# Performance work log

Measured on AMD Instinct MI355X. Metric: run time of the kernel, lower is better.

Reference implementation:

```python
import jax, jax.numpy as jnp
import numpy as np

B, N, D, H, PD, HID = 16, 512, 512, 8, 9, 32
DH = D // H


def setup_inputs() -> dict:
    key = jax.random.key(0)
    ks = jax.random.split(key, 8)
    h = jax.random.normal(ks[0], (B, N, D), dtype=jnp.float32)
    v = jax.random.normal(ks[1], (B, N, 4), dtype=jnp.float32)
    m = jax.random.randint(ks[2], (B, N), 0, 2, dtype=jnp.int32)
    token_type_ids = jax.random.randint(ks[3], (N,), 0, 4, dtype=jnp.int32)
    s = 1.0 / np.sqrt(D)
    W_qkv = jax.random.normal(ks[4], (D, 3 * D), dtype=jnp.float32) * s
    W_out = jax.random.normal(ks[5], (D, D), dtype=jnp.float32) * s
    W1 = jax.random.normal(ks[6], (PD, HID), dtype=jnp.float32) * (1.0 / np.sqrt(PD))
    b1 = jnp.zeros((HID,), dtype=jnp.float32)
    W2 = jax.random.normal(ks[7], (HID, H), dtype=jnp.float32) * (1.0 / np.sqrt(HID))
    b2 = jnp.zeros((H,), dtype=jnp.float32)
    return {"h": h, "v": v, "m": m, "token_type_ids": token_type_ids,
            "W_qkv": W_qkv, "W_out": W_out, "W1": W1, "b1": b1, "W2": W2, "b2": b2}


def build_pairwise_features(v, token_type_ids):
    # v: [B,N,4] -> e: [B,N,N,9] = [v_i - v_j (4), v_i * v_j (4), same_type (1)]
    vi = v[:, :, None, :]
    vj = v[:, None, :, :]
    same = (token_type_ids[:, None] == token_type_ids[None, :]).astype(v.dtype)
    same = jnp.broadcast_to(same[None, :, :, None], v.shape[:1] + same.shape + (1,))
    return jnp.concatenate([vi - vj, vi * vj, same], axis=-1)


def reference(h, v, m, token_type_ids, W_qkv, W_out, W1, b1, W2, b2):
    Bq, Nq, Dq = h.shape
    qkv = h @ W_qkv                                    # [B,N,3D]
    q, k, vv = jnp.split(qkv, 3, axis=-1)
    def heads(x):
        return x.reshape(Bq, Nq, H, DH).transpose(0, 2, 1, 3)  # [B,H,N,dh]
    q, k, vv = heads(q), heads(k), heads(vv)
    logits = jnp.einsum('bhid,bhjd->bhij', q, k) / jnp.sqrt(jnp.float32(DH))
    e = build_pairwise_features(v, token_type_ids)     # [B,N,N,9]
    bias = jax.nn.relu(e @ W1 + b1) @ W2 + b2          # [B,N,N,H]
    logits = logits + bias.transpose(0, 3, 1, 2)       # [B,H,N,N]
    key_invalid = (m == 0)[:, None, None, :]           # [B,1,1,N]
    logits = jnp.where(key_invalid, -jnp.inf, logits)
    attn = jax.nn.softmax(logits, axis=-1)             # dropout is identity (p=0/eval)
    out = jnp.einsum('bhij,bhjd->bhid', attn, vv)
    out = out.transpose(0, 2, 1, 3).reshape(Bq, Nq, Dq) @ W_out
    out = out * (m != 0).astype(out.dtype)[:, :, None]
    return out
```

## Files before the change

kernel.cpp:

```cpp
#include <hip/hip_runtime.h>
#include <hip/hip_bf16.h>
#include <hip/hip_fp16.h>

#define NN 512
#define HH 8
#define DHH 64

typedef __attribute__((ext_vector_type(8))) short short8v;
typedef __attribute__((ext_vector_type(8))) unsigned short ushort8v;
typedef __attribute__((ext_vector_type(4))) unsigned short ushort4v;
typedef __attribute__((ext_vector_type(4))) float f32x4;
typedef __attribute__((ext_vector_type(8))) _Float16 f16x8;
typedef __attribute__((ext_vector_type(4))) _Float16 f16x4;

__device__ __forceinline__ unsigned short f2bf(float x) {
  unsigned u = __builtin_bit_cast(unsigned, x);
  u += 0x7FFFu + ((u >> 16) & 1u);
  return (unsigned short)(u >> 16);
}
__device__ __forceinline__ int swz64(int r, int cb) { return r * 64 + (cb ^ (((r >> 1) & 3) << 4)); }
__device__ __forceinline__ int swz128(int r, int cb) { return r * 128 + (cb ^ ((r & 7) << 4)); }

__global__ __launch_bounds__(256) void cvt_bf(const float* __restrict__ src,
                                              unsigned short* __restrict__ dst, int n) {
  int i = (blockIdx.x * 256 + threadIdx.x) * 4;
  if (i < n) {
    float4 v = *(const float4*)&src[i];
    ushort4v o;
    o[0] = f2bf(v.x); o[1] = f2bf(v.y); o[2] = f2bf(v.z); o[3] = f2bf(v.w);
    *(ushort4v*)&dst[i] = o;
  }
}

__global__ __launch_bounds__(256) void transpose_cvt(const float* __restrict__ src,
                                                     unsigned short* __restrict__ dst,
                                                     int R, int C) {
  __shared__ float t[32][33];
  const int r0 = blockIdx.x * 32, c0 = blockIdx.y * 32;
  const int rr = threadIdx.x >> 3, c4 = (threadIdx.x & 7) * 4;
  float4 v = *(const float4*)&src[(size_t)(r0 + rr) * C + c0 + c4];
  t[rr][c4 + 0] = v.x; t[rr][c4 + 1] = v.y; t[rr][c4 + 2] = v.z; t[rr][c4 + 3] = v.w;
  __syncthreads();
  ushort4v o;
#pragma unroll
  for (int e = 0; e < 4; ++e) o[e] = f2bf(t[c4 + e][rr]);
  *(ushort4v*)&dst[(size_t)(c0 + rr) * R + r0 + c4] = o;
}

__device__ __forceinline__ void gemm128_body(const unsigned short* __restrict__ A,
                                             const unsigned short* __restrict__ Bt,
                                             int ldk, int m0, int n0,
                                             f32x4 acc[4][4], unsigned char* smem) {
  const int tid = threadIdx.x, lane = tid & 63, wid = tid >> 6;
  const int wm = wid >> 1, wn = wid & 1;
  int aoff[4], boff[4];
#pragma unroll
  for (int i = 0; i < 4; ++i) {
    aoff[i] = swz64(wm * 64 + i * 16 + (lane & 15), (lane >> 4) * 16);
    boff[i] = 8192 + swz64(wn * 64 + i * 16 + (lane & 15), (lane >> 4) * 16);
  }
  for (int k0 = 0; k0 < ldk; k0 += 32) {
#pragma unroll
    for (int p = 0; p < 2; ++p) {
      const int idx = p * 256 + tid;
      const int r = idx >> 2, cg = idx & 3;
      ushort8v av = *(const ushort8v*)&A[(size_t)(m0 + r) * ldk + k0 + cg * 8];
      *(ushort8v*)&smem[swz64(r, cg * 16)] = av;
      ushort8v bv = *(const ushort8v*)&Bt[(size_t)(n0 + r) * ldk + k0 + cg * 8];
      *(ushort8v*)&smem[8192 + swz64(r, cg * 16)] = bv;
    }
    __syncthreads();
    short8v a[4], b[4];
#pragma unroll
    for (int i = 0; i < 4; ++i) {
      a[i] = *(const short8v*)&smem[aoff[i]];
      b[i] = *(const short8v*)&smem[boff[i]];
    }
#pragma unroll
    for (int i = 0; i < 4; ++i)
#pragma unroll
      for (int j = 0; j < 4; ++j)
        acc[i][j] = __builtin_amdgcn_mfma_f32_16x16x32_bf16(a[i], b[j], acc[i][j], 0, 0, 0);
    __syncthreads();
  }
}

__global__ __launch_bounds__(256) void gemm_qkv(const unsigned short* __restrict__ A,
                                                const unsigned short* __restrict__ Bt,
                                                unsigned short* __restrict__ q,
                                                unsigned short* __restrict__ k,
                                                unsigned short* __restrict__ v) {
  __shared__ unsigned char smem[16384];
  f32x4 acc[4][4];
  const f32x4 z = {0.f, 0.f, 0.f, 0.f};
#pragma unroll
  for (int i = 0; i < 4; ++i)
#pragma unroll
    for (int j = 0; j < 4; ++j) acc[i][j] = z;
  gemm128_body(A, Bt, 512, blockIdx.x * 128, blockIdx.y * 128, acc, smem);
  const int lane = threadIdx.x & 63, wid = threadIdx.x >> 6;
  const int wm = wid >> 1, wn = wid & 1;
#pragma unroll
  for (int i = 0; i < 4; ++i) {
    const int row0 = blockIdx.x * 128 + wm * 64 + i * 16 + ((lane >> 4) << 2);
#pragma unroll
    for (int j = 0; j < 4; ++j) {
      const int col = blockIdx.y * 128 + wn * 64 + j * 16 + (lane & 15);
      const int part = col >> 9, head = (col >> 6) & 7, dh = col & 63;
      unsigned short* dst = (part == 0) ? q : ((part == 1) ? k : v);
#pragma unroll
      for (int rr = 0; rr < 4; ++rr) {
        const int row = row0 + rr;
        const int b_ = row >> 9, n_ = row & 511;
        dst[(((b_ * HH + head) * NN) + n_) * DHH + dh] = f2bf(acc[i][j][rr]);
      }
    }
  }
}

__global__ __launch_bounds__(256) void gemm_out(const unsigned short* __restrict__ A,
                                                const unsigned short* __restrict__ Bt,
                                                const int* __restrict__ msk,
                                                float* __restrict__ out) {
  __shared__ unsigned char smem[16384];
  f32x4 acc[4][4];
  const f32x4 z = {0.f, 0.f, 0.f, 0.f};
#pragma unroll
  for (int i = 0; i < 4; ++i)
#pragma unroll
    for (int j = 0; j < 4; ++j) acc[i][j] = z;
  gemm128_body(A, Bt, 512, blockIdx.x * 128, blockIdx.y * 128, acc, smem);
  const int lane = threadIdx.x & 63, wid = threadIdx.x >> 6;
  const int wm = wid >> 1, wn = wid & 1;
#pragma unroll
  for (int i = 0; i < 4; ++i) {
    const int row0 = blockIdx.x * 128 + wm * 64 + i * 16 + ((lane >> 4) << 2);
#pragma unroll
    for (int j = 0; j < 4; ++j) {
      const int col = blockIdx.y * 128 + wn * 64 + j * 16 + (lane & 15);
#pragma unroll
      for (int rr = 0; rr < 4; ++rr) {
        const int row = row0 + rr;
        const float mm = (msk[row] != 0) ? 1.f : 0.f;
        out[(size_t)row * 512 + col] = acc[i][j][rr] * mm;
      }
    }
  }
}

__global__ __launch_bounds__(256) void bias_mlp_mfma(
    const float* __restrict__ v, const int* __restrict__ tti,
    const float* __restrict__ W1, const float* __restrict__ b1,
    const float* __restrict__ W2, const float* __restrict__ b2,
    __half* __restrict__ bias) {
  __shared__ float sv[NN][4];
  __shared__ int stt[NN];
  __shared__ _Float16 hbuf[4][16 * 40];
  const int tid = threadIdx.x, lane = tid & 63, w = tid >> 6;
  const int i = blockIdx.x, b = blockIdx.y;
  const int l16 = lane & 15, lg = lane >> 4;
  for (int idx = tid; idx < NN; idx += 256) {
    *(float4*)&sv[idx][0] = *(const float4*)&v[(b * NN + idx) * 4];
    stt[idx] = tti[idx];
  }
  f16x8 w1f[2], w2f;
#pragma unroll
  for (int t = 0; t < 2; ++t)
#pragma unroll
    for (int e = 0; e < 8; ++e) {
      const int kk = lg * 8 + e;
      w1f[t][e] = (kk < 9) ? (_Float16)W1[kk * 32 + t * 16 + l16] : (_Float16)0.f;
    }
#pragma unroll
  for (int e = 0; e < 8; ++e)
    w2f[e] = (l16 < 8) ? (_Float16)W2[(lg * 8 + e) * 8 + l16] : (_Float16)0.f;
  const float b1v0 = b1[l16], b1v1 = b1[16 + l16];
  const float b2v = (l16 < 8) ? b2[l16] : 0.f;
  __syncthreads();
  const float4 vi = *(const float4*)&sv[i][0];
  const int ti = stt[i];
  _Float16* hb = &hbuf[w][0];
  for (int j0 = w * 16; j0 < NN; j0 += 64) {
    const int j = j0 + l16;
    const float4 vj = *(const float4*)&sv[j][0];
    f16x8 af = {0, 0, 0, 0, 0, 0, 0, 0};
    if (lg == 0) {
      af[0] = (_Float16)(vi.x - vj.x); af[1] = (_Float16)(vi.y - vj.y);
      af[2] = (_Float16)(vi.z - vj.z); af[3] = (_Float16)(vi.w - vj.w);
      af[4] = (_Float16)(vi.x * vj.x); af[5] = (_Float16)(vi.y * vj.y);
      af[6] = (_Float16)(vi.z * vj.z); af[7] = (_Float16)(vi.w * vj.w);
    } else if (lg == 1) {
      af[0] = (ti == stt[j]) ? (_Float16)1.f : (_Float16)0.f;
    }
    f32x4 h0 = {b1v0, b1v0, b1v0, b1v0};
    f32x4 h1 = {b1v1, b1v1, b1v1, b1v1};
    h0 = __builtin_amdgcn_mfma_f32_16x16x32_f16(af, w1f[0], h0, 0, 0, 0);
    h1 = __builtin_amdgcn_mfma_f32_16x16x32_f16(af, w1f[1], h1, 0, 0, 0);
#pragma unroll
    for (int r = 0; r < 4; ++r) {
      const int row = lg * 4 + r;
      hb[row * 40 + l16] = (_Float16)fmaxf(h0[r], 0.f);
      hb[row * 40 + 16 + l16] = (_Float16)fmaxf(h1[r], 0.f);
    }
    f16x8 af2 = *(const f16x8*)&hb[l16 * 40 + lg * 8];
    f32x4 o = {b2v, b2v, b2v, b2v};
    o = __builtin_amdgcn_mfma_f32_16x16x32_f16(af2, w2f, o, 0, 0, 0);
    if (l16 < 8) {
      f16x4 pk;
#pragma unroll
      for (int r = 0; r < 4; ++r) pk[r] = (_Float16)o[r];
      *(f16x4*)&bias[((size_t)(b * HH + l16) * NN + i) * NN + j0 + lg * 4] = pk;
    }
  }
}

__global__ __launch_bounds__(256) void attn_mfma(
    const unsigned short* __restrict__ q, const unsigned short* __restrict__ k,
    const unsigned short* __restrict__ v, const __half* __restrict__ bias,
    const int* __restrict__ msk, unsigned short* __restrict__ ao) {
  __shared__ unsigned char vt[8192];
  __shared__ unsigned char ps[4][2048];
  __shared__ float smask[NN];
  const int tid = threadIdx.x, lane = tid & 63, w = tid >> 6;
  const int it = blockIdx.x, h_ = blockIdx.y, b_ = blockIdx.z;
  const int bh = b_ * HH + h_;
  const unsigned short* qb = q + ((size_t)bh * NN + it * 64) * DHH;
  const unsigned short* kb = k + (size_t)bh * NN * DHH;
  const unsigned short* vb = v + (size_t)bh * NN * DHH;
  const __half* bb = bias + (size_t)bh * NN * NN;
  for (int j = tid; j < NN; j += 256) smask[j] = (msk[b_ * NN + j] != 0) ? 0.f : -1e30f;
  short8v qf[2];
#pragma unroll
  for (int kc = 0; kc < 2; ++kc)
    qf[kc] = *(const short8v*)&qb[(w * 16 + (lane & 15)) * DHH + kc * 32 + (lane >> 4) * 8];
  f32x4 acc[4];
  const f32x4 z = {0.f, 0.f, 0.f, 0.f};
#pragma unroll
  for (int d = 0; d < 4; ++d) acc[d] = z;
  float mrow[4], lrow[4];
#pragma unroll
  for (int r = 0; r < 4; ++r) { mrow[r] = -1e30f; lrow[r] = 0.f; }
  __syncthreads();
  const int irow_base = it * 64 + w * 16 + ((lane >> 4) << 2);
  for (int j0 = 0; j0 < NN; j0 += 64) {
#pragma unroll
    for (int p = 0; p < 2; ++p) {
      const int idx = p * 256 + tid;
      const int j = idx & 63, dh0 = (idx >> 6) * 8;
      ushort8v v8 = *(const ushort8v*)&vb[(j0 + j) * DHH + dh0];
#pragma unroll
      for (int e = 0; e < 8; ++e)
        *(unsigned short*)&vt[swz128(dh0 + e, 2 * j)] = v8[e];
    }
    f32x4 s[4];
#pragma unroll
    for (int jt = 0; jt < 4; ++jt) {
      const unsigned short* kr = &kb[(j0 + jt * 16 + (lane & 15)) * DHH + (lane >> 4) * 8];
      short8v kf0 = *(const short8v*)&kr[0];
      short8v kf1 = *(const short8v*)&kr[32];
      f32x4 t = z;
      t = __builtin_amdgcn_mfma_f32_16x16x32_bf16(qf[0], kf0, t, 0, 0, 0);
      t = __builtin_amdgcn_mfma_f32_16x16x32_bf16(qf[1], kf1, t, 0, 0, 0);
      s[jt] = t;
    }
#pragma unroll
    for (int jt = 0; jt < 4; ++jt) {
      const int jcol = j0 + jt * 16 + (lane & 15);
#pragma unroll
      for (int r = 0; r < 4; ++r) {
        const float bv = __half2float(bb[(size_t)(irow_base + r) * NN + jcol]);
        s[jt][r] = fmaf(s[jt][r], 0.125f, bv) + smask[jcol];
      }
    }
    float alpha[4];
#pragma unroll
    for (int r = 0; r < 4; ++r) {
      float tm = fmaxf(fmaxf(s[0][r], s[1][r]), fmaxf(s[2][r], s[3][r]));
      tm = fmaxf(tm, __shfl_xor(tm, 1));
      tm = fmaxf(tm, __shfl_xor(tm, 2));
      tm = fmaxf(tm, __shfl_xor(tm, 4));
      tm = fmaxf(tm, __shfl_xor(tm, 8));
      const float mn = fmaxf(mrow[r], tm);
      alpha[r] = __expf(mrow[r] - mn);
      mrow[r] = mn;
      float ts = 0.f;
#pragma unroll
      for (int jt = 0; jt < 4; ++jt) {
        const float p = __expf(s[jt][r] - mn);
        s[jt][r] = p;
        ts += p;
      }
      ts += __shfl_xor(ts, 1);
      ts += __shfl_xor(ts, 2);
      ts += __shfl_xor(ts, 4);
      ts += __shfl_xor(ts, 8);
      lrow[r] = lrow[r] * alpha[r] + ts;
    }
#pragma unroll
    for (int d = 0; d < 4; ++d)
#pragma unroll
      for (int r = 0; r < 4; ++r) acc[d][r] *= alpha[r];
#pragma unroll
    for (int jt = 0; jt < 4; ++jt)
#pragma unroll
      for (int r = 0; r < 4; ++r)
        *(unsigned short*)&ps[w][swz128(((lane >> 4) << 2) + r, jt * 32 + 2 * (lane & 15))] =
            f2bf(s[jt][r]);
    __syncthreads();
    short8v pf[2];
#pragma unroll
    for (int kc = 0; kc < 2; ++kc)
      pf[kc] = *(const short8v*)&ps[w][swz128(lane & 15, kc * 64 + (lane >> 4) * 16)];
#pragma unroll
    for (int d = 0; d < 4; ++d) {
      short8v vf0 = *(const short8v*)&vt[swz128(d * 16 + (lane & 15), (lane >> 4) * 16)];
      short8v vf1 = *(const short8v*)&vt[swz128(d * 16 + (lane & 15), 64 + (lane >> 4) * 16)];
      acc[d] = __builtin_amdgcn_mfma_f32_16x16x32_bf16(pf[0], vf0, acc[d], 0, 0, 0);
      acc[d] = __builtin_amdgcn_mfma_f32_16x16x32_bf16(pf[1], vf1, acc[d], 0, 0, 0);
    }
    __syncthreads();
  }
#pragma unroll
  for (int d = 0; d < 4; ++d) {
#pragma unroll
    for (int r = 0; r < 4; ++r) {
      const int row = irow_base + r;
      ao[(size_t)(b_ * NN + row) * 512 + h_ * DHH + d * 16 + (lane & 15)] =
          f2bf(acc[d][r] / lrow[r]);
    }
  }
}

extern "C" void kernel_launch(void* const* d_in, const int* in_sizes, int n_in,
                              void* d_out, int out_size, void* d_ws, size_t ws_size,
                              hipStream_t stream) {
  const float* h     = (const float*)d_in[0];
  const float* v     = (const float*)d_in[1];
  const int*   m     = (const int*)d_in[2];
  const int*   tti   = (const int*)d_in[3];
  const float* W_qkv = (const float*)d_in[4];
  const float* W_out = (const float*)d_in[5];
  const float* W1    = (const float*)d_in[6];
  const float* b1    = (const float*)d_in[7];
  const float* W2    = (const float*)d_in[8];
  const float* b2    = (const float*)d_in[9];
  float* out = (float*)d_out;
  unsigned char* ws = (unsigned char*)d_ws;

  unsigned short* h_bf  = (unsigned short*)(ws + 0);
  unsigned short* q_bf  = (unsigned short*)(ws + 8388608);
  unsigned short* k_bf  = (unsigned short*)(ws + 16777216);
  unsigned short* v_bf  = (unsigned short*)(ws + 25165824);
  unsigned short* ao_bf = (unsigned short*)(ws + 33554432);
  unsigned short* WqT   = (unsigned short*)(ws + 41943040);
  unsigned short* WoT   = (unsigned short*)(ws + 43515904);
  __half* bias          = (__half*)(ws + 44040192);

  cvt_bf<<<4096, 256, 0, stream>>>(h, h_bf, 16 * NN * 512);
  transpose_cvt<<<dim3(16, 48), 256, 0, stream>>>(W_qkv, WqT, 512, 1536);
  transpose_cvt<<<dim3(16, 16), 256, 0, stream>>>(W_out, WoT, 512, 512);
  gemm_qkv<<<dim3(64, 12), 256, 0, stream>>>(h_bf, WqT, q_bf, k_bf, v_bf);
  bias_mlp_mfma<<<dim3(512, 16), 256, 0, stream>>>(v, tti, W1, b1, W2, b2, bias);
  attn_mfma<<<dim3(8, 8, 16), 256, 0, stream>>>(q_bf, k_bf, v_bf, bias, m, ao_bf);
  gemm_out<<<dim3(64, 4), 256, 0, stream>>>(ao_bf, WoT, m, out);
}
```

Measured before the change: 151.3 us.

## Fuse pairwise bias MLP into attention kernel and store V transposed

```diff
diff --git a/kernel.cpp b/kernel.cpp
--- a/kernel.cpp
+++ b/kernel.cpp
@@ -89,7 +89,7 @@
                                                 const unsigned short* __restrict__ Bt,
                                                 unsigned short* __restrict__ q,
                                                 unsigned short* __restrict__ k,
-                                                unsigned short* __restrict__ v) {
+                                                unsigned short* __restrict__ vt) {
   __shared__ unsigned char smem[16384];
   f32x4 acc[4][4];
   const f32x4 z = {0.f, 0.f, 0.f, 0.f};
@@ -107,12 +107,17 @@
     for (int j = 0; j < 4; ++j) {
       const int col = blockIdx.y * 128 + wn * 64 + j * 16 + (lane & 15);
       const int part = col >> 9, head = (col >> 6) & 7, dh = col & 63;
-      unsigned short* dst = (part == 0) ? q : ((part == 1) ? k : v);
 #pragma unroll
       for (int rr = 0; rr < 4; ++rr) {
         const int row = row0 + rr;
         const int b_ = row >> 9, n_ = row & 511;
-        dst[(((b_ * HH + head) * NN) + n_) * DHH + dh] = f2bf(acc[i][j][rr]);
+        const unsigned short val = f2bf(acc[i][j][rr]);
+        if (part == 0)
+          q[(((b_ * HH + head) * NN) + n_) * DHH + dh] = val;
+        else if (part == 1)
+          k[(((b_ * HH + head) * NN) + n_) * DHH + dh] = val;
+        else
+          vt[(((b_ * HH + head) * DHH) + dh) * NN + n_] = val;
       }
     }
   }
@@ -148,20 +153,27 @@
   }
 }
 
-__global__ __launch_bounds__(256) void bias_mlp_mfma(
-    const float* __restrict__ v, const int* __restrict__ tti,
+__global__ __launch_bounds__(512, 4) void attn_bias_fused(
+    const unsigned short* __restrict__ q, const unsigned short* __restrict__ k,
+    const unsigned short* __restrict__ vt, const float* __restrict__ vvec,
+    const int* __restrict__ tti, const int* __restrict__ msk,
     const float* __restrict__ W1, const float* __restrict__ b1,
     const float* __restrict__ W2, const float* __restrict__ b2,
-    __half* __restrict__ bias) {
+    unsigned short* __restrict__ ao) {
   __shared__ float sv[NN][4];
   __shared__ int stt[NN];
-  __shared__ _Float16 hbuf[4][16 * 40];
+  __shared__ float smask[NN];
+  __shared__ _Float16 bias_lds[2][HH][16][68];
+  __shared__ _Float16 hbuf[HH][16 * 40];
+  __shared__ unsigned char ps[HH][2048];
   const int tid = threadIdx.x, lane = tid & 63, w = tid >> 6;
-  const int i = blockIdx.x, b = blockIdx.y;
   const int l16 = lane & 15, lg = lane >> 4;
-  for (int idx = tid; idx < NN; idx += 256) {
-    *(float4*)&sv[idx][0] = *(const float4*)&v[(b * NN + idx) * 4];
+  const int it = blockIdx.x, b_ = blockIdx.y;
+  const int i0 = it * 16;
+  for (int idx = tid; idx < NN; idx += 512) {
+    *(float4*)&sv[idx][0] = *(const float4*)&vvec[(b_ * NN + idx) * 4];
     stt[idx] = tti[idx];
+    smask[idx] = (msk[b_ * NN + idx] != 0) ? 0.f : -1e30f;
   }
   f16x8 w1f[2], w2f;
 #pragma unroll
@@ -176,63 +188,13 @@
     w2f[e] = (l16 < 8) ? (_Float16)W2[(lg * 8 + e) * 8 + l16] : (_Float16)0.f;
   const float b1v0 = b1[l16], b1v1 = b1[16 + l16];
   const float b2v = (l16 < 8) ? b2[l16] : 0.f;
-  __syncthreads();
-  const float4 vi = *(const float4*)&sv[i][0];
-  const int ti = stt[i];
-  _Float16* hb = &hbuf[w][0];
-  for (int j0 = w * 16; j0 < NN; j0 += 64) {
-    const int j = j0 + l16;
-    const float4 vj = *(const float4*)&sv[j][0];
-    f16x8 af = {0, 0, 0, 0, 0, 0, 0, 0};
-    if (lg == 0) {
-      af[0] = (_Float16)(vi.x - vj.x); af[1] = (_Float16)(vi.y - vj.y);
-      af[2] = (_Float16)(vi.z - vj.z); af[3] = (_Float16)(vi.w - vj.w);
-      af[4] = (_Float16)(vi.x * vj.x); af[5] = (_Float16)(vi.y * vj.y);
-      af[6] = (_Float16)(vi.z * vj.z); af[7] = (_Float16)(vi.w * vj.w);
-    } else if (lg == 1) {
-      af[0] = (ti == stt[j]) ? (_Float16)1.f : (_Float16)0.f;
-    }
-    f32x4 h0 = {b1v0, b1v0, b1v0, b1v0};
-    f32x4 h1 = {b1v1, b1v1, b1v1, b1v1};
-    h0 = __builtin_amdgcn_mfma_f32_16x16x32_f16(af, w1f[0], h0, 0, 0, 0);
-    h1 = __builtin_amdgcn_mfma_f32_16x16x32_f16(af, w1f[1], h1, 0, 0, 0);
-#pragma unroll
-    for (int r = 0; r < 4; ++r) {
-      const int row = lg * 4 + r;
-      hb[row * 40 + l16] = (_Float16)fmaxf(h0[r], 0.f);
-      hb[row * 40 + 16 + l16] = (_Float16)fmaxf(h1[r], 0.f);
-    }
-    f16x8 af2 = *(const f16x8*)&hb[l16 * 40 + lg * 8];
-    f32x4 o = {b2v, b2v, b2v, b2v};
-    o = __builtin_amdgcn_mfma_f32_16x16x32_f16(af2, w2f, o, 0, 0, 0);
-    if (l16 < 8) {
-      f16x4 pk;
-#pragma unroll
-      for (int r = 0; r < 4; ++r) pk[r] = (_Float16)o[r];
-      *(f16x4*)&bias[((size_t)(b * HH + l16) * NN + i) * NN + j0 + lg * 4] = pk;
-    }
-  }
-}
-
-__global__ __launch_bounds__(256) void attn_mfma(
-    const unsigned short* __restrict__ q, const unsigned short* __restrict__ k,
-    const unsigned short* __restrict__ v, const __half* __restrict__ bias,
-    const int* __restrict__ msk, unsigned short* __restrict__ ao) {
-  __shared__ unsigned char vt[8192];
-  __shared__ unsigned char ps[4][2048];
-  __shared__ float smask[NN];
-  const int tid = threadIdx.x, lane = tid & 63, w = tid >> 6;
-  const int it = blockIdx.x, h_ = blockIdx.y, b_ = blockIdx.z;
-  const int bh = b_ * HH + h_;
-  const unsigned short* qb = q + ((size_t)bh * NN + it * 64) * DHH;
-  const unsigned short* kb = k + (size_t)bh * NN * DHH;
-  const unsigned short* vb = v + (size_t)bh * NN * DHH;
-  const __half* bb = bias + (size_t)bh * NN * NN;
-  for (int j = tid; j < NN; j += 256) smask[j] = (msk[b_ * NN + j] != 0) ? 0.f : -1e30f;
+  const unsigned short* qb = q + ((size_t)(b_ * HH + w) * NN + i0) * DHH;
+  const unsigned short* kb = k + (size_t)(b_ * HH + w) * NN * DHH;
+  const unsigned short* vtb = vt + (size_t)(b_ * HH + w) * DHH * NN;
   short8v qf[2];
 #pragma unroll
   for (int kc = 0; kc < 2; ++kc)
-    qf[kc] = *(const short8v*)&qb[(w * 16 + (lane & 15)) * DHH + kc * 32 + (lane >> 4) * 8];
+    qf[kc] = *(const short8v*)&qb[l16 * DHH + kc * 32 + lg * 8];
   f32x4 acc[4];
   const f32x4 z = {0.f, 0.f, 0.f, 0.f};
 #pragma unroll
@@ -240,22 +202,50 @@
   float mrow[4], lrow[4];
 #pragma unroll
   for (int r = 0; r < 4; ++r) { mrow[r] = -1e30f; lrow[r] = 0.f; }
+  _Float16* hb = &hbuf[w][0];
   __syncthreads();
-  const int irow_base = it * 64 + w * 16 + ((lane >> 4) << 2);
+  int pbuf = 0;
   for (int j0 = 0; j0 < NN; j0 += 64) {
-#pragma unroll
-    for (int p = 0; p < 2; ++p) {
-      const int idx = p * 256 + tid;
-      const int j = idx & 63, dh0 = (idx >> 6) * 8;
-      ushort8v v8 = *(const ushort8v*)&vb[(j0 + j) * DHH + dh0];
-#pragma unroll
-      for (int e = 0; e < 8; ++e)
-        *(unsigned short*)&vt[swz128(dh0 + e, 2 * j)] = v8[e];
-    }
+    for (int tt = 0; tt < 8; ++tt) {
+      const int il = w * 2 + (tt >> 2), jg = tt & 3;
+      const float4 vi = *(const float4*)&sv[i0 + il][0];
+      const int ti = stt[i0 + il];
+      const int j = j0 + jg * 16 + l16;
+      const float4 vj = *(const float4*)&sv[j][0];
+      f16x8 af = {0, 0, 0, 0, 0, 0, 0, 0};
+      if (lg == 0) {
+        af[0] = (_Float16)(vi.x - vj.x); af[1] = (_Float16)(vi.y - vj.y);
+        af[2] = (_Float16)(vi.z - vj.z); af[3] = (_Float16)(vi.w - vj.w);
+        af[4] = (_Float16)(vi.x * vj.x); af[5] = (_Float16)(vi.y * vj.y);
+        af[6] = (_Float16)(vi.z * vj.z); af[7] = (_Float16)(vi.w * vj.w);
+      } else if (lg == 1) {
+        af[0] = (ti == stt[j]) ? (_Float16)1.f : (_Float16)0.f;
+      }
+      f32x4 h0 = {b1v0, b1v0, b1v0, b1v0};
+      f32x4 h1 = {b1v1, b1v1, b1v1, b1v1};
+      h0 = __builtin_amdgcn_mfma_f32_16x16x32_f16(af, w1f[0], h0, 0, 0, 0);
+      h1 = __builtin_amdgcn_mfma_f32_16x16x32_f16(af, w1f[1], h1, 0, 0, 0);
+#pragma unroll
+      for (int r = 0; r < 4; ++r) {
+        const int row = lg * 4 + r;
+        hb[row * 40 + l16] = (_Float16)fmaxf(h0[r], 0.f);
+        hb[row * 40 + 16 + l16] = (_Float16)fmaxf(h1[r], 0.f);
+      }
+      f16x8 af2 = *(const f16x8*)&hb[l16 * 40 + lg * 8];
+      f32x4 o = {b2v, b2v, b2v, b2v};
+      o = __builtin_amdgcn_mfma_f32_16x16x32_f16(af2, w2f, o, 0, 0, 0);
+      if (l16 < 8) {
+        f16x4 pk;
+#pragma unroll
+        for (int r = 0; r < 4; ++r) pk[r] = (_Float16)o[r];
+        *(f16x4*)&bias_lds[pbuf][l16][il][jg * 16 + lg * 4] = pk;
+      }
+    }
+    __syncthreads();
     f32x4 s[4];
 #pragma unroll
     for (int jt = 0; jt < 4; ++jt) {
-      const unsigned short* kr = &kb[(j0 + jt * 16 + (lane & 15)) * DHH + (lane >> 4) * 8];
+      const unsigned short* kr = &kb[(j0 + jt * 16 + l16) * DHH + lg * 8];
       short8v kf0 = *(const short8v*)&kr[0];
       short8v kf1 = *(const short8v*)&kr[32];
       f32x4 t = z;
@@ -265,11 +255,12 @@
     }
 #pragma unroll
     for (int jt = 0; jt < 4; ++jt) {
-      const int jcol = j0 + jt * 16 + (lane & 15);
+      const int jcol = j0 + jt * 16 + l16;
+      const float mk = smask[jcol];
 #pragma unroll
       for (int r = 0; r < 4; ++r) {
-        const float bv = __half2float(bb[(size_t)(irow_base + r) * NN + jcol]);
-        s[jt][r] = fmaf(s[jt][r], 0.125f, bv) + smask[jcol];
+        const float bv = (float)bias_lds[pbuf][w][lg * 4 + r][jt * 16 + l16];
+        s[jt][r] = fmaf(s[jt][r], 0.125f, bv) + mk;
       }
     }
     float alpha[4];
@@ -304,28 +295,27 @@
     for (int jt = 0; jt < 4; ++jt)
 #pragma unroll
       for (int r = 0; r < 4; ++r)
-        *(unsigned short*)&ps[w][swz128(((lane >> 4) << 2) + r, jt * 32 + 2 * (lane & 15))] =
-            f2bf(s[jt][r]);
-    __syncthreads();
+        *(unsigned short*)&ps[w][swz128(lg * 4 + r, jt * 32 + 2 * l16)] = f2bf(s[jt][r]);
     short8v pf[2];
 #pragma unroll
     for (int kc = 0; kc < 2; ++kc)
-      pf[kc] = *(const short8v*)&ps[w][swz128(lane & 15, kc * 64 + (lane >> 4) * 16)];
+      pf[kc] = *(const short8v*)&ps[w][swz128(l16, kc * 64 + lg * 16)];
 #pragma unroll
     for (int d = 0; d < 4; ++d) {
-      short8v vf0 = *(const short8v*)&vt[swz128(d * 16 + (lane & 15), (lane >> 4) * 16)];
-      short8v vf1 = *(const short8v*)&vt[swz128(d * 16 + (lane & 15), 64 + (lane >> 4) * 16)];
+      const unsigned short* vr = &vtb[(size_t)(d * 16 + l16) * NN + j0 + lg * 8];
+      short8v vf0 = *(const short8v*)&vr[0];
+      short8v vf1 = *(const short8v*)&vr[32];
       acc[d] = __builtin_amdgcn_mfma_f32_16x16x32_bf16(pf[0], vf0, acc[d], 0, 0, 0);
       acc[d] = __builtin_amdgcn_mfma_f32_16x16x32_bf16(pf[1], vf1, acc[d], 0, 0, 0);
     }
-    __syncthreads();
+    pbuf ^= 1;
   }
 #pragma unroll
   for (int d = 0; d < 4; ++d) {
 #pragma unroll
     for (int r = 0; r < 4; ++r) {
-      const int row = irow_base + r;
-      ao[(size_t)(b_ * NN + row) * 512 + h_ * DHH + d * 16 + (lane & 15)] =
+      const int row = i0 + lg * 4 + r;
+      ao[(size_t)(b_ * NN + row) * 512 + w * DHH + d * 16 + l16] =
           f2bf(acc[d][r] / lrow[r]);
     }
   }
@@ -350,17 +340,16 @@
   unsigned short* h_bf  = (unsigned short*)(ws + 0);
   unsigned short* q_bf  = (unsigned short*)(ws + 8388608);
   unsigned short* k_bf  = (unsigned short*)(ws + 16777216);
-  unsigned short* v_bf  = (unsigned short*)(ws + 25165824);
+  unsigned short* vt_bf = (unsigned short*)(ws + 25165824);
   unsigned short* ao_bf = (unsigned short*)(ws + 33554432);
   unsigned short* WqT   = (unsigned short*)(ws + 41943040);
   unsigned short* WoT   = (unsigned short*)(ws + 43515904);
-  __half* bias          = (__half*)(ws + 44040192);
 
   cvt_bf<<<4096, 256, 0, stream>>>(h, h_bf, 16 * NN * 512);
   transpose_cvt<<<dim3(16, 48), 256, 0, stream>>>(W_qkv, WqT, 512, 1536);
   transpose_cvt<<<dim3(16, 16), 256, 0, stream>>>(W_out, WoT, 512, 512);
-  gemm_qkv<<<dim3(64, 12), 256, 0, stream>>>(h_bf, WqT, q_bf, k_bf, v_bf);
-  bias_mlp_mfma<<<dim3(512, 16), 256, 0, stream>>>(v, tti, W1, b1, W2, b2, bias);
-  attn_mfma<<<dim3(8, 8, 16), 256, 0, stream>>>(q_bf, k_bf, v_bf, bias, m, ao_bf);
+  gemm_qkv<<<dim3(64, 12), 256, 0, stream>>>(h_bf, WqT, q_bf, k_bf, vt_bf);
+  attn_bias_fused<<<dim3(32, 16), 512, 0, stream>>>(q_bf, k_bf, vt_bf, v, tti, m,
+                                                    W1, b1, W2, b2, ao_bf);
   gemm_out<<<dim3(64, 4), 256, 0, stream>>>(ao_bf, WoT, m, out);
 }
```

Result: no change. 154.3 us (+2.0%).

## Store V transposed from QKV GEMM and compute S^T in attention

Applied to the files above, without the earlier changes.

```diff
diff --git a/kernel.cpp b/kernel.cpp
--- a/kernel.cpp
+++ b/kernel.cpp
@@ -89,7 +89,7 @@
                                                 const unsigned short* __restrict__ Bt,
                                                 unsigned short* __restrict__ q,
                                                 unsigned short* __restrict__ k,
-                                                unsigned short* __restrict__ v) {
+                                                unsigned short* __restrict__ vt) {
   __shared__ unsigned char smem[16384];
   f32x4 acc[4][4];
   const f32x4 z = {0.f, 0.f, 0.f, 0.f};
@@ -107,12 +107,20 @@
     for (int j = 0; j < 4; ++j) {
       const int col = blockIdx.y * 128 + wn * 64 + j * 16 + (lane & 15);
       const int part = col >> 9, head = (col >> 6) & 7, dh = col & 63;
-      unsigned short* dst = (part == 0) ? q : ((part == 1) ? k : v);
-#pragma unroll
-      for (int rr = 0; rr < 4; ++rr) {
-        const int row = row0 + rr;
-        const int b_ = row >> 9, n_ = row & 511;
-        dst[(((b_ * HH + head) * NN) + n_) * DHH + dh] = f2bf(acc[i][j][rr]);
+      if (part == 2) {
+        const int b_ = row0 >> 9, n_ = row0 & 511;
+        ushort4v pk;
+#pragma unroll
+        for (int rr = 0; rr < 4; ++rr) pk[rr] = f2bf(acc[i][j][rr]);
+        *(ushort4v*)&vt[(((b_ * HH + head) * DHH) + dh) * NN + n_] = pk;
+      } else {
+        unsigned short* dst = (part == 0) ? q : k;
+#pragma unroll
+        for (int rr = 0; rr < 4; ++rr) {
+          const int row = row0 + rr;
+          const int b_ = row >> 9, n_ = row & 511;
+          dst[(((b_ * HH + head) * NN) + n_) * DHH + dh] = f2bf(acc[i][j][rr]);
+        }
       }
     }
   }
@@ -214,119 +222,114 @@
   }
 }
 
-__global__ __launch_bounds__(256) void attn_mfma(
+__global__ __launch_bounds__(256) void attn_mfma2(
     const unsigned short* __restrict__ q, const unsigned short* __restrict__ k,
-    const unsigned short* __restrict__ v, const __half* __restrict__ bias,
+    const unsigned short* __restrict__ vt, const __half* __restrict__ bias,
     const int* __restrict__ msk, unsigned short* __restrict__ ao) {
-  __shared__ unsigned char vt[8192];
+  __shared__ float smask[NN];
   __shared__ unsigned char ps[4][2048];
-  __shared__ float smask[NN];
   const int tid = threadIdx.x, lane = tid & 63, w = tid >> 6;
+  const int l16 = lane & 15, lg = lane >> 4;
   const int it = blockIdx.x, h_ = blockIdx.y, b_ = blockIdx.z;
   const int bh = b_ * HH + h_;
-  const unsigned short* qb = q + ((size_t)bh * NN + it * 64) * DHH;
+  const int i_wave = it * 64 + w * 16;
+  const unsigned short* qb = q + ((size_t)bh * NN + i_wave) * DHH;
   const unsigned short* kb = k + (size_t)bh * NN * DHH;
-  const unsigned short* vb = v + (size_t)bh * NN * DHH;
-  const __half* bb = bias + (size_t)bh * NN * NN;
+  const unsigned short* vtb = vt + (size_t)bh * DHH * NN;
+  const __half* brow = bias + ((size_t)bh * NN + (i_wave + l16)) * NN;
   for (int j = tid; j < NN; j += 256) smask[j] = (msk[b_ * NN + j] != 0) ? 0.f : -1e30f;
+  __syncthreads();
   short8v qf[2];
 #pragma unroll
   for (int kc = 0; kc < 2; ++kc)
-    qf[kc] = *(const short8v*)&qb[(w * 16 + (lane & 15)) * DHH + kc * 32 + (lane >> 4) * 8];
+    qf[kc] = *(const short8v*)&qb[l16 * DHH + kc * 32 + lg * 8];
   f32x4 acc[4];
   const f32x4 z = {0.f, 0.f, 0.f, 0.f};
 #pragma unroll
   for (int d = 0; d < 4; ++d) acc[d] = z;
-  float mrow[4], lrow[4];
-#pragma unroll
-  for (int r = 0; r < 4; ++r) { mrow[r] = -1e30f; lrow[r] = 0.f; }
-  __syncthreads();
-  const int irow_base = it * 64 + w * 16 + ((lane >> 4) << 2);
+  float mrow = -1e30f, lrow = 0.f;
+  unsigned char* psw = &ps[w][0];
   for (int j0 = 0; j0 < NN; j0 += 64) {
-#pragma unroll
-    for (int p = 0; p < 2; ++p) {
-      const int idx = p * 256 + tid;
-      const int j = idx & 63, dh0 = (idx >> 6) * 8;
-      ushort8v v8 = *(const ushort8v*)&vb[(j0 + j) * DHH + dh0];
-#pragma unroll
-      for (int e = 0; e < 8; ++e)
-        *(unsigned short*)&vt[swz128(dh0 + e, 2 * j)] = v8[e];
-    }
     f32x4 s[4];
 #pragma unroll
     for (int jt = 0; jt < 4; ++jt) {
-      const unsigned short* kr = &kb[(j0 + jt * 16 + (lane & 15)) * DHH + (lane >> 4) * 8];
+      const unsigned short* kr = &kb[(j0 + jt * 16 + l16) * DHH + lg * 8];
       short8v kf0 = *(const short8v*)&kr[0];
       short8v kf1 = *(const short8v*)&kr[32];
       f32x4 t = z;
-      t = __builtin_amdgcn_mfma_f32_16x16x32_bf16(qf[0], kf0, t, 0, 0, 0);
-      t = __builtin_amdgcn_mfma_f32_16x16x32_bf16(qf[1], kf1, t, 0, 0, 0);
+      t = __builtin_amdgcn_mfma_f32_16x16x32_bf16(kf0, qf[0], t, 0, 0, 0);
+      t = __builtin_amdgcn_mfma_f32_16x16x32_bf16(kf1, qf[1], t, 0, 0, 0);
       s[jt] = t;
     }
 #pragma unroll
     for (int jt = 0; jt < 4; ++jt) {
-      const int jcol = j0 + jt * 16 + (lane & 15);
+      const int jb = j0 + jt * 16 + lg * 4;
+      const f16x4 bv = *(const f16x4*)&brow[jb];
+      const float4 mk = *(const float4*)&smask[jb];
+      s[jt][0] = fmaf(s[jt][0], 0.125f, (float)bv[0]) + mk.x;
+      s[jt][1] = fmaf(s[jt][1], 0.125f, (float)bv[1]) + mk.y;
+      s[jt][2] = fmaf(s[jt][2], 0.125f, (float)bv[2]) + mk.z;
+      s[jt][3] = fmaf(s[jt][3], 0.125f, (float)bv[3]) + mk.w;
+    }
+    float tm = -1e30f;
+#pragma unroll
+    for (int jt = 0; jt < 4; ++jt)
+#pragma unroll
+      for (int r = 0; r < 4; ++r) tm = fmaxf(tm, s[jt][r]);
+    tm = fmaxf(tm, __shfl_xor(tm, 16));
+    tm = fmaxf(tm, __shfl_xor(tm, 32));
+    const float mn = fmaxf(mrow, tm);
+    const float alpha = __expf(mrow - mn);
+    mrow = mn;
+    float ts = 0.f;
+#pragma unroll
+    for (int jt = 0; jt < 4; ++jt)
 #pragma unroll
       for (int r = 0; r < 4; ++r) {
-        const float bv = __half2float(bb[(size_t)(irow_base + r) * NN + jcol]);
-        s[jt][r] = fmaf(s[jt][r], 0.125f, bv) + smask[jcol];
-      }
-    }
-    float alpha[4];
-#pragma unroll
-    for (int r = 0; r < 4; ++r) {
-      float tm = fmaxf(fmaxf(s[0][r], s[1][r]), fmaxf(s[2][r], s[3][r]));
-      tm = fmaxf(tm, __shfl_xor(tm, 1));
-      tm = fmaxf(tm, __shfl_xor(tm, 2));
-      tm = fmaxf(tm, __shfl_xor(tm, 4));
-      tm = fmaxf(tm, __shfl_xor(tm, 8));
-      const float mn = fmaxf(mrow[r], tm);
-      alpha[r] = __expf(mrow[r] - mn);
-      mrow[r] = mn;
-      float ts = 0.f;
-#pragma unroll
-      for (int jt = 0; jt < 4; ++jt) {
         const float p = __expf(s[jt][r] - mn);
         s[jt][r] = p;
         ts += p;
       }
-      ts += __shfl_xor(ts, 1);
-      ts += __shfl_xor(ts, 2);
-      ts += __shfl_xor(ts, 4);
-      ts += __shfl_xor(ts, 8);
-      lrow[r] = lrow[r] * alpha[r] + ts;
-    }
+    ts += __shfl_xor(ts, 16);
+    ts += __shfl_xor(ts, 32);
+    lrow = lrow * alpha + ts;
+    float a4[4];
+#pragma unroll
+    for (int r = 0; r < 4; ++r) a4[r] = __shfl(alpha, (lg << 2) + r);
 #pragma unroll
     for (int d = 0; d < 4; ++d)
 #pragma unroll
-      for (int r = 0; r < 4; ++r) acc[d][r] *= alpha[r];
-#pragma unroll
-    for (int jt = 0; jt < 4; ++jt)
-#pragma unroll
-      for (int r = 0; r < 4; ++r)
-        *(unsigned short*)&ps[w][swz128(((lane >> 4) << 2) + r, jt * 32 + 2 * (lane & 15))] =
-            f2bf(s[jt][r]);
-    __syncthreads();
+      for (int r = 0; r < 4; ++r) acc[d][r] *= a4[r];
+#pragma unroll
+    for (int jt = 0; jt < 4; ++jt) {
+      ushort4v pk;
+#pragma unroll
+      for (int r = 0; r < 4; ++r) pk[r] = f2bf(s[jt][r]);
+      *(ushort4v*)&psw[swz128(l16, jt * 32 + lg * 8)] = pk;
+    }
     short8v pf[2];
 #pragma unroll
     for (int kc = 0; kc < 2; ++kc)
-      pf[kc] = *(const short8v*)&ps[w][swz128(lane & 15, kc * 64 + (lane >> 4) * 16)];
+      pf[kc] = *(const short8v*)&psw[swz128(l16, kc * 64 + lg * 16)];
 #pragma unroll
     for (int d = 0; d < 4; ++d) {
-      short8v vf0 = *(const short8v*)&vt[swz128(d * 16 + (lane & 15), (lane >> 4) * 16)];
-      short8v vf1 = *(const short8v*)&vt[swz128(d * 16 + (lane & 15), 64 + (lane >> 4) * 16)];
+      const unsigned short* vr = &vtb[(size_t)(d * 16 + l16) * NN + j0 + lg * 8];
+      short8v vf0 = *(const short8v*)&vr[0];
+      short8v vf1 = *(const short8v*)&vr[32];
       acc[d] = __builtin_amdgcn_mfma_f32_16x16x32_bf16(pf[0], vf0, acc[d], 0, 0, 0);
       acc[d] = __builtin_amdgcn_mfma_f32_16x16x32_bf16(pf[1], vf1, acc[d], 0, 0, 0);
     }
-    __syncthreads();
-  }
+  }
+  float lr4[4];
+#pragma unroll
+  for (int r = 0; r < 4; ++r) lr4[r] = __shfl(lrow, (lg << 2) + r);
 #pragma unroll
   for (int d = 0; d < 4; ++d) {
 #pragma unroll
     for (int r = 0; r < 4; ++r) {
-      const int row = irow_base + r;
-      ao[(size_t)(b_ * NN + row) * 512 + h_ * DHH + d * 16 + (lane & 15)] =
-          f2bf(acc[d][r] / lrow[r]);
+      const int row = i_wave + (lg << 2) + r;
+      ao[(size_t)(b_ * NN + row) * 512 + h_ * DHH + d * 16 + l16] =
+          f2bf(acc[d][r] / lr4[r]);
     }
   }
 }
@@ -350,7 +353,7 @@
   unsigned short* h_bf  = (unsigned short*)(ws + 0);
   unsigned short* q_bf  = (unsigned short*)(ws + 8388608);
   unsigned short* k_bf  = (unsigned short*)(ws + 16777216);
-  unsigned short* v_bf  = (unsigned short*)(ws + 25165824);
+  unsigned short* vt_bf = (unsigned short*)(ws + 25165824);
   unsigned short* ao_bf = (unsigned short*)(ws + 33554432);
   unsigned short* WqT   = (unsigned short*)(ws + 41943040);
   unsigned short* WoT   = (unsigned short*)(ws + 43515904);
@@ -359,8 +362,8 @@
   cvt_bf<<<4096, 256, 0, stream>>>(h, h_bf, 16 * NN * 512);
   transpose_cvt<<<dim3(16, 48), 256, 0, stream>>>(W_qkv, WqT, 512, 1536);
   transpose_cvt<<<dim3(16, 16), 256, 0, stream>>>(W_out, WoT, 512, 512);
-  gemm_qkv<<<dim3(64, 12), 256, 0, stream>>>(h_bf, WqT, q_bf, k_bf, v_bf);
+  gemm_qkv<<<dim3(64, 12), 256, 0, stream>>>(h_bf, WqT, q_bf, k_bf, vt_bf);
   bias_mlp_mfma<<<dim3(512, 16), 256, 0, stream>>>(v, tti, W1, b1, W2, b2, bias);
-  attn_mfma<<<dim3(8, 8, 16), 256, 0, stream>>>(q_bf, k_bf, v_bf, bias, m, ao_bf);
+  attn_mfma2<<<dim3(8, 8, 16), 256, 0, stream>>>(q_bf, k_bf, vt_bf, bias, m, ao_bf);
   gemm_out<<<dim3(64, 4), 256, 0, stream>>>(ao_bf, WoT, m, out);
 }
```

Result: slower. 212.0 us (+40.1%).
